# Performance work log

Measured on AMD Instinct MI355X. Metric: run time of the kernel, lower is better.

The kernel has to match this reference:

```python
import math
import jax, jax.numpy as jnp
import numpy as np

B, T, C, H = 2, 4096, 512, 8  # batch, seq_len, n_embd, n_head
D = C // H                    # head_dim = 64

def setup_inputs() -> dict:
    key = jax.random.key(0)
    k1, k2, k3 = jax.random.split(key, 3)
    x = jax.random.normal(k1, (B, T, C), dtype=jnp.float32)
    # torch Linear(C, 3C, bias=False): y = x @ W.T; we store the transposed
    # weight directly so the forward is x @ W_attn.
    W_attn = jax.random.normal(k2, (C, 3 * C), dtype=jnp.float32) * 0.02
    W_proj = jax.random.normal(k3, (C, C), dtype=jnp.float32) * 0.02
    return {"x": x, "W_attn": W_attn, "W_proj": W_proj}

def reference(x, W_attn, W_proj):
    b, t, c = x.shape
    # fused QKV projection, split like .split(n_embd, dim=2)
    qkv = x @ W_attn                              # [B,T,3C]
    q, k, v = jnp.split(qkv, 3, axis=-1)          # each [B,T,C]
    def to_heads(u):
        return u.reshape(b, t, H, D).transpose(0, 2, 1, 3)  # [B,H,T,D]
    q, k, v = to_heads(q), to_heads(k), to_heads(v)
    scale = 1.0 / math.sqrt(D)
    att = jnp.einsum('bhqd,bhkd->bhqk', q, k) * scale       # [B,H,T,T]
    causal = jnp.tril(jnp.ones((t, t), dtype=bool))         # masked_fill(triu(...,1), -inf)
    att = jnp.where(causal, att, -jnp.inf)
    probs = jax.nn.softmax(att, axis=-1)
    y = jnp.einsum('bhqk,bhkd->bhqd', probs, v)             # [B,H,T,D]
    y = y.transpose(0, 2, 1, 3).reshape(b, t, c)            # [B,T,C]
    return y @ W_proj
```

## Files before the change

kernel.cpp:

```cpp
#include <hip/hip_runtime.h>
#include <hip/hip_bf16.h>
#include <stdint.h>


typedef __attribute__((ext_vector_type(8))) short short8;
typedef __attribute__((ext_vector_type(4))) float floatx4;

__device__ __forceinline__ unsigned short f2bf(float f) {
    unsigned int x = __float_as_uint(f);
    unsigned int r = x + 0x7fffu + ((x >> 16) & 1u);
    return (unsigned short)(r >> 16);
}

__global__ __launch_bounds__(256) void convert_x(
    const float* __restrict__ x, unsigned short* __restrict__ xb)
{
    size_t i = ((size_t)blockIdx.x * 256 + threadIdx.x) * 8;
    float4 a = *reinterpret_cast<const float4*>(x + i);
    float4 b = *reinterpret_cast<const float4*>(x + i + 4);
    unsigned short o[8] = {f2bf(a.x), f2bf(a.y), f2bf(a.z), f2bf(a.w),
                           f2bf(b.x), f2bf(b.y), f2bf(b.z), f2bf(b.w)};
    *reinterpret_cast<uint4*>(xb + i) = *reinterpret_cast<uint4*>(o);
}

__global__ __launch_bounds__(256) void transpose_w(
    const float* __restrict__ W, unsigned short* __restrict__ Wt, int Kdim, int Ndim)
{
    __shared__ unsigned short tile[32][34];
    const int tid = threadIdx.x;
    const int tx = tid & 31, ty = tid >> 5;
    const int n0 = blockIdx.x * 32, k0 = blockIdx.y * 32;
    #pragma unroll
    for (int p = 0; p < 4; ++p) {
        int k = k0 + ty + p * 8;
        tile[tx][ty + p * 8] = f2bf(W[(size_t)k * Ndim + n0 + tx]);
    }
    __syncthreads();
    #pragma unroll
    for (int p = 0; p < 4; ++p) {
        int n = n0 + ty + p * 8;
        Wt[(size_t)n * Kdim + k0 + tx] = tile[ty + p * 8][tx];
    }
}

template<int EPI>
__global__ __launch_bounds__(256) void mm_bt(
    const unsigned short* __restrict__ A,
    const unsigned short* __restrict__ Bt,
    void* __restrict__ outp)
{
    __shared__ __align__(16) unsigned short Al[128][40];
    __shared__ __align__(16) unsigned short Bl[128][40];

    const int tid  = threadIdx.x;
    const int wave = tid >> 6;
    const int lane = tid & 63;
    const int quad = lane >> 4;
    const int l16  = lane & 15;
    const int wr   = wave >> 1;
    const int wc   = wave & 1;
    const int n0 = blockIdx.x * 128;
    const int m0 = blockIdx.y * 128;

    floatx4 acc[4][4];
    #pragma unroll
    for (int i = 0; i < 4; ++i)
        #pragma unroll
        for (int j = 0; j < 4; ++j) acc[i][j] = (floatx4){0.f, 0.f, 0.f, 0.f};

    const int row = tid >> 1;
    const int cb  = (tid & 1) * 16;

    const unsigned short* ap = &A[(size_t)(m0 + row) * 512 + cb];
    const unsigned short* bp = &Bt[(size_t)(n0 + row) * 512 + cb];

    uint4 ra0 = *reinterpret_cast<const uint4*>(ap);
    uint4 ra1 = *reinterpret_cast<const uint4*>(ap + 8);
    uint4 rb0 = *reinterpret_cast<const uint4*>(bp);
    uint4 rb1 = *reinterpret_cast<const uint4*>(bp + 8);

    for (int k0 = 0; k0 < 512; k0 += 32) {
        __syncthreads();
        *reinterpret_cast<uint4*>(&Al[row][cb])     = ra0;
        *reinterpret_cast<uint4*>(&Al[row][cb + 8]) = ra1;
        *reinterpret_cast<uint4*>(&Bl[row][cb])     = rb0;
        *reinterpret_cast<uint4*>(&Bl[row][cb + 8]) = rb1;
        __syncthreads();

        if (k0 < 480) {
            ra0 = *reinterpret_cast<const uint4*>(ap + k0 + 32);
            ra1 = *reinterpret_cast<const uint4*>(ap + k0 + 40);
            rb0 = *reinterpret_cast<const uint4*>(bp + k0 + 32);
            rb1 = *reinterpret_cast<const uint4*>(bp + k0 + 40);
        }

        short8 af[4], bf[4];
        #pragma unroll
        for (int ti = 0; ti < 4; ++ti)
            af[ti] = *reinterpret_cast<const short8*>(&Al[wr * 64 + ti * 16 + l16][quad * 8]);
        #pragma unroll
        for (int tj = 0; tj < 4; ++tj)
            bf[tj] = *reinterpret_cast<const short8*>(&Bl[wc * 64 + tj * 16 + l16][quad * 8]);
        #pragma unroll
        for (int ti = 0; ti < 4; ++ti)
            #pragma unroll
            for (int tj = 0; tj < 4; ++tj)
                acc[ti][tj] = __builtin_amdgcn_mfma_f32_16x16x32_bf16(af[ti], bf[tj], acc[ti][tj], 0, 0, 0);
    }

    if (EPI == 0) {
        unsigned short* WS = (unsigned short*)outp;
        unsigned short* Qb  = WS;
        unsigned short* Kb  = WS + 4194304;
        unsigned short* Vtb = WS + 8388608;
        const int which = n0 >> 9;
        const int h = ((n0 + wc * 64) >> 6) & 7;
        const float sc = (which == 0) ? 0.18033688f : 1.0f;
        #pragma unroll
        for (int ti = 0; ti < 4; ++ti) {
            #pragma unroll
            for (int r = 0; r < 4; ++r) {
                int m = m0 + wr * 64 + ti * 16 + quad * 4 + r;
                int b = m >> 12, t = m & 4095;
                int bh = b * 8 + h;
                #pragma unroll
                for (int tj = 0; tj < 4; ++tj) {
                    int d = tj * 16 + l16;
                    unsigned short val = f2bf(acc[ti][tj][r] * sc);
                    if (which == 0)      Qb[((size_t)bh * 4096 + t) * 64 + d] = val;
                    else if (which == 1) Kb[((size_t)bh * 4096 + t) * 64 + d] = val;
                    else                 Vtb[((size_t)bh * 64 + d) * 4096 + t] = val;
                }
            }
        }
    } else {
        float* Out = (float*)outp;
        #pragma unroll
        for (int ti = 0; ti < 4; ++ti) {
            #pragma unroll
            for (int r = 0; r < 4; ++r) {
                int m = m0 + wr * 64 + ti * 16 + quad * 4 + r;
                #pragma unroll
                for (int tj = 0; tj < 4; ++tj) {
                    int n = n0 + wc * 64 + tj * 16 + l16;
                    Out[(size_t)m * 512 + n] = acc[ti][tj][r];
                }
            }
        }
    }
}

__global__ __launch_bounds__(256) void attn_mfma(
    const unsigned short* __restrict__ Q,
    const unsigned short* __restrict__ K,
    const unsigned short* __restrict__ Vt,
    unsigned short* __restrict__ Y)
{
    __shared__ __align__(16) unsigned short Kc[64][72];
    __shared__ __align__(16) unsigned short Vc[64][72];
    __shared__ __align__(16) unsigned short Pc[4][32][72];

    const int tid  = threadIdx.x;
    const int wave = tid >> 6;
    const int lane = tid & 63;
    const int quad = lane >> 4;
    const int l16  = lane & 15;

    const int bid = blockIdx.x;
    const int bh = bid & 15;
    const int j  = (bid >> 4) & 15;
    const int g  = bid >> 8;
    const int qb = g ? (31 - j) : j;
    const int m0 = qb * 128;

    const unsigned short* Qp = Q  + (size_t)bh * (4096 * 64);
    const unsigned short* Kp = K  + (size_t)bh * (4096 * 64);
    const unsigned short* Vp = Vt + (size_t)bh * (64 * 4096);

    short8 qf[2][2];
    #pragma unroll
    for (int h = 0; h < 2; ++h) {
        int qrow = m0 + wave * 32 + h * 16 + l16;
        qf[h][0] = *reinterpret_cast<const short8*>(&Qp[(size_t)qrow * 64 + quad * 8]);
        qf[h][1] = *reinterpret_cast<const short8*>(&Qp[(size_t)qrow * 64 + 32 + quad * 8]);
    }

    short8 ones;
    #pragma unroll
    for (int i = 0; i < 8; ++i) ones[i] = (short)0x3F80;

    floatx4 o[2][4];
    #pragma unroll
    for (int h = 0; h < 2; ++h)
        #pragma unroll
        for (int n = 0; n < 4; ++n) o[h][n] = (floatx4){0.f, 0.f, 0.f, 0.f};
    floatx4 o4[2] = {{0,0,0,0},{0,0,0,0}};

    const int r0 = tid >> 3, c0 = (tid & 7) * 8;
    const int r1 = r0 + 32,  c1 = c0;
    const int ktmax = 2 * qb + 1;
    const int wq0 = m0 + wave * 32;

    uint4 rk0 = *reinterpret_cast<const uint4*>(&Kp[(size_t)r0 * 64 + c0]);
    uint4 rk1 = *reinterpret_cast<const uint4*>(&Kp[(size_t)r1 * 64 + c1]);
    uint4 rv0 = *reinterpret_cast<const uint4*>(&Vp[(size_t)r0 * 4096 + c0]);
    uint4 rv1 = *reinterpret_cast<const uint4*>(&Vp[(size_t)r1 * 4096 + c1]);

    for (int kt = 0; kt <= ktmax; ++kt) {
        __syncthreads();
        *reinterpret_cast<uint4*>(&Kc[r0][c0]) = rk0;
        *reinterpret_cast<uint4*>(&Kc[r1][c1]) = rk1;
        *reinterpret_cast<uint4*>(&Vc[r0][c0]) = rv0;
        *reinterpret_cast<uint4*>(&Vc[r1][c1]) = rv1;
        __syncthreads();

        if (kt < ktmax) {
            const int jn = (kt + 1) * 64;
            rk0 = *reinterpret_cast<const uint4*>(&Kp[(size_t)(jn + r0) * 64 + c0]);
            rk1 = *reinterpret_cast<const uint4*>(&Kp[(size_t)(jn + r1) * 64 + c1]);
            rv0 = *reinterpret_cast<const uint4*>(&Vp[(size_t)r0 * 4096 + jn + c0]);
            rv1 = *reinterpret_cast<const uint4*>(&Vp[(size_t)r1 * 4096 + jn + c1]);
        }

        if (kt * 64 > wq0 + 31) continue;

        float sv[2][4][4];
        #pragma unroll
        for (int ct = 0; ct < 4; ++ct) {
            short8 a0 = *reinterpret_cast<const short8*>(&Kc[ct * 16 + l16][quad * 8]);
            short8 a1 = *reinterpret_cast<const short8*>(&Kc[ct * 16 + l16][32 + quad * 8]);
            floatx4 s0 = {0, 0, 0, 0}, s1 = {0, 0, 0, 0};
            s0 = __builtin_amdgcn_mfma_f32_16x16x32_bf16(a0, qf[0][0], s0, 0, 0, 0);
            s0 = __builtin_amdgcn_mfma_f32_16x16x32_bf16(a1, qf[0][1], s0, 0, 0, 0);
            s1 = __builtin_amdgcn_mfma_f32_16x16x32_bf16(a0, qf[1][0], s1, 0, 0, 0);
            s1 = __builtin_amdgcn_mfma_f32_16x16x32_bf16(a1, qf[1][1], s1, 0, 0, 0);
            #pragma unroll
            for (int r = 0; r < 4; ++r) { sv[0][ct][r] = s0[r]; sv[1][ct][r] = s1[r]; }
        }

        if (kt * 64 + 63 > wq0) {
            #pragma unroll
            for (int h = 0; h < 2; ++h)
                #pragma unroll
                for (int ct = 0; ct < 4; ++ct)
                    #pragma unroll
                    for (int r = 0; r < 4; ++r) {
                        int key = kt * 64 + ct * 16 + quad * 4 + r;
                        int q   = wq0 + h * 16 + l16;
                        sv[h][ct][r] = (key <= q) ? sv[h][ct][r] : -1e30f;
                    }
        }
        #pragma unroll
        for (int h = 0; h < 2; ++h)
            #pragma unroll
            for (int ct = 0; ct < 4; ++ct)
                #pragma unroll
                for (int r = 0; r < 4; ++r)
                    sv[h][ct][r] = __builtin_amdgcn_exp2f(sv[h][ct][r]);

        #pragma unroll
        for (int h = 0; h < 2; ++h)
            #pragma unroll
            for (int ct = 0; ct < 4; ++ct) {
                unsigned int d0 = (unsigned int)f2bf(sv[h][ct][0]) | ((unsigned int)f2bf(sv[h][ct][1]) << 16);
                unsigned int d1 = (unsigned int)f2bf(sv[h][ct][2]) | ((unsigned int)f2bf(sv[h][ct][3]) << 16);
                *reinterpret_cast<uint2*>(&Pc[wave][h * 16 + l16][ct * 16 + quad * 4]) = make_uint2(d0, d1);
            }

        short8 pa[2][2];
        #pragma unroll
        for (int h = 0; h < 2; ++h) {
            pa[h][0] = *reinterpret_cast<const short8*>(&Pc[wave][h * 16 + l16][quad * 8]);
            pa[h][1] = *reinterpret_cast<const short8*>(&Pc[wave][h * 16 + l16][32 + quad * 8]);
        }

        #pragma unroll
        for (int h = 0; h < 2; ++h) {
            o4[h] = __builtin_amdgcn_mfma_f32_16x16x32_bf16(pa[h][0], ones, o4[h], 0, 0, 0);
            o4[h] = __builtin_amdgcn_mfma_f32_16x16x32_bf16(pa[h][1], ones, o4[h], 0, 0, 0);
        }
        #pragma unroll
        for (int n = 0; n < 4; ++n) {
            short8 b0 = *reinterpret_cast<const short8*>(&Vc[n * 16 + l16][quad * 8]);
            short8 b1 = *reinterpret_cast<const short8*>(&Vc[n * 16 + l16][32 + quad * 8]);
            #pragma unroll
            for (int h = 0; h < 2; ++h) {
                o[h][n] = __builtin_amdgcn_mfma_f32_16x16x32_bf16(pa[h][0], b0, o[h][n], 0, 0, 0);
                o[h][n] = __builtin_amdgcn_mfma_f32_16x16x32_bf16(pa[h][1], b1, o[h][n], 0, 0, 0);
            }
        }
    }

    const int b = bh >> 3, h8 = bh & 7;
    #pragma unroll
    for (int h = 0; h < 2; ++h)
        #pragma unroll
        for (int r = 0; r < 4; ++r) {
            float inv = 1.0f / o4[h][r];
            int t = wq0 + h * 16 + quad * 4 + r;
            #pragma unroll
            for (int n = 0; n < 4; ++n)
                Y[((size_t)(b * 4096 + t)) * 512 + h8 * 64 + n * 16 + l16] = f2bf(o[h][n][r] * inv);
        }
}

extern "C" void kernel_launch(void* const* d_in, const int* in_sizes, int n_in,
                              void* d_out, int out_size, void* d_ws, size_t ws_size,
                              hipStream_t stream) {
    const float* x  = (const float*)d_in[0];
    const float* Wa = (const float*)d_in[1];
    const float* Wp = (const float*)d_in[2];
    float* out = (float*)d_out;
    unsigned short* ws = (unsigned short*)d_ws;

    unsigned short* Qb  = ws;
    unsigned short* Kb  = ws + 4194304;
    unsigned short* Vtb = ws + 8388608;
    unsigned short* Yb  = ws + 12582912;
    unsigned short* WaT = Yb;
    unsigned short* WpT = Qb;
    unsigned short* xb  = (unsigned short*)d_out;

    dim3 blk(256);
    convert_x<<<dim3(2048), blk, 0, stream>>>(x, xb);
    transpose_w<<<dim3(48, 16), blk, 0, stream>>>(Wa, WaT, 512, 1536);
    mm_bt<0><<<dim3(12, 64), blk, 0, stream>>>(xb, WaT, (void*)ws);
    attn_mfma<<<dim3(512), blk, 0, stream>>>(Qb, Kb, Vtb, Yb);
    transpose_w<<<dim3(16, 16), blk, 0, stream>>>(Wp, WpT, 512, 512);
    mm_bt<1><<<dim3(4, 64), blk, 0, stream>>>(Yb, WpT, (void*)out);
}
```

Before: 196.4 us.

## Fuse prep kernels, stage V-transpose via LDS, and shrink attention blocks to 64 queries

The x conversion and W_attn transpose are merged into one launch. The QKV GEMM grid is reordered so M varies fastest, and the V epilogue now transposes through shared memory to write coalesced 16-byte rows instead of scattered 2-byte stores. Attention blocks drop to 2 waves covering 64 queries, giving 1024 blocks with the longest-first ordering. Each wave then does only useful key tiles, with masking confined to the diagonal tile. The costs are a larger LDS footprint for the QKV GEMM and more K/V reloads per query across the smaller blocks.

```diff
diff --git a/kernel.cpp b/kernel.cpp
--- a/kernel.cpp
+++ b/kernel.cpp
@@ -12,35 +12,48 @@
     return (unsigned short)(r >> 16);
 }
 
-__global__ __launch_bounds__(256) void convert_x(
-    const float* __restrict__ x, unsigned short* __restrict__ xb)
+__global__ __launch_bounds__(256) void prep_a(
+    const float* __restrict__ x, unsigned short* __restrict__ xb,
+    const float* __restrict__ Wa, unsigned short* __restrict__ WaT)
 {
-    size_t i = ((size_t)blockIdx.x * 256 + threadIdx.x) * 8;
-    float4 a = *reinterpret_cast<const float4*>(x + i);
-    float4 b = *reinterpret_cast<const float4*>(x + i + 4);
-    unsigned short o[8] = {f2bf(a.x), f2bf(a.y), f2bf(a.z), f2bf(a.w),
-                           f2bf(b.x), f2bf(b.y), f2bf(b.z), f2bf(b.w)};
-    *reinterpret_cast<uint4*>(xb + i) = *reinterpret_cast<uint4*>(o);
-}
-
-__global__ __launch_bounds__(256) void transpose_w(
-    const float* __restrict__ W, unsigned short* __restrict__ Wt, int Kdim, int Ndim)
+    const int bid = blockIdx.x;
+    const int tid = threadIdx.x;
+    if (bid < 2048) {
+        size_t i = ((size_t)bid * 256 + tid) * 8;
+        float4 a = *reinterpret_cast<const float4*>(x + i);
+        float4 b = *reinterpret_cast<const float4*>(x + i + 4);
+        unsigned short o[8] = {f2bf(a.x), f2bf(a.y), f2bf(a.z), f2bf(a.w),
+                               f2bf(b.x), f2bf(b.y), f2bf(b.z), f2bf(b.w)};
+        *reinterpret_cast<uint4*>(xb + i) = *reinterpret_cast<uint4*>(o);
+    } else {
+        __shared__ unsigned short tile[32][34];
+        const int t2 = bid - 2048;
+        const int n0 = (t2 % 48) * 32, k0 = (t2 / 48) * 32;
+        const int tx = tid & 31, ty = tid >> 5;
+        #pragma unroll
+        for (int p = 0; p < 4; ++p)
+            tile[tx][ty + p * 8] = f2bf(Wa[(size_t)(k0 + ty + p * 8) * 1536 + n0 + tx]);
+        __syncthreads();
+        #pragma unroll
+        for (int p = 0; p < 4; ++p)
+            WaT[(size_t)(n0 + ty + p * 8) * 512 + k0 + tx] = tile[ty + p * 8][tx];
+    }
+}
+
+__global__ __launch_bounds__(256) void transpose_wp(
+    const float* __restrict__ W, unsigned short* __restrict__ Wt)
 {
     __shared__ unsigned short tile[32][34];
     const int tid = threadIdx.x;
     const int tx = tid & 31, ty = tid >> 5;
     const int n0 = blockIdx.x * 32, k0 = blockIdx.y * 32;
     #pragma unroll
-    for (int p = 0; p < 4; ++p) {
-        int k = k0 + ty + p * 8;
-        tile[tx][ty + p * 8] = f2bf(W[(size_t)k * Ndim + n0 + tx]);
-    }
+    for (int p = 0; p < 4; ++p)
+        tile[tx][ty + p * 8] = f2bf(W[(size_t)(k0 + ty + p * 8) * 512 + n0 + tx]);
     __syncthreads();
     #pragma unroll
-    for (int p = 0; p < 4; ++p) {
-        int n = n0 + ty + p * 8;
-        Wt[(size_t)n * Kdim + k0 + tx] = tile[ty + p * 8][tx];
-    }
+    for (int p = 0; p < 4; ++p)
+        Wt[(size_t)(n0 + ty + p * 8) * 512 + k0 + tx] = tile[ty + p * 8][tx];
 }
 
 template<int EPI>
@@ -49,8 +62,9 @@
     const unsigned short* __restrict__ Bt,
     void* __restrict__ outp)
 {
-    __shared__ __align__(16) unsigned short Al[128][40];
-    __shared__ __align__(16) unsigned short Bl[128][40];
+    __shared__ __align__(16) unsigned char smem[EPI == 0 ? 40960 : 20480];
+    auto Al = reinterpret_cast<unsigned short(*)[40]>(smem);
+    auto Bl = reinterpret_cast<unsigned short(*)[40]>(smem + 10240);
 
     const int tid  = threadIdx.x;
     const int wave = tid >> 6;
@@ -59,8 +73,8 @@
     const int l16  = lane & 15;
     const int wr   = wave >> 1;
     const int wc   = wave & 1;
-    const int n0 = blockIdx.x * 128;
-    const int m0 = blockIdx.y * 128;
+    const int m0 = blockIdx.x * 128;
+    const int n0 = blockIdx.y * 128;
 
     floatx4 acc[4][4];
     #pragma unroll
@@ -115,21 +129,47 @@
         unsigned short* Vtb = WS + 8388608;
         const int which = n0 >> 9;
         const int h = ((n0 + wc * 64) >> 6) & 7;
-        const float sc = (which == 0) ? 0.18033688f : 1.0f;
-        #pragma unroll
-        for (int ti = 0; ti < 4; ++ti) {
-            #pragma unroll
-            for (int r = 0; r < 4; ++r) {
-                int m = m0 + wr * 64 + ti * 16 + quad * 4 + r;
-                int b = m >> 12, t = m & 4095;
-                int bh = b * 8 + h;
+
+        if (which == 2) {
+            auto Tr = reinterpret_cast<unsigned short(*)[80]>(smem);
+            __syncthreads();
+            #pragma unroll
+            for (int ti = 0; ti < 4; ++ti)
                 #pragma unroll
                 for (int tj = 0; tj < 4; ++tj) {
-                    int d = tj * 16 + l16;
-                    unsigned short val = f2bf(acc[ti][tj][r] * sc);
-                    if (which == 0)      Qb[((size_t)bh * 4096 + t) * 64 + d] = val;
-                    else if (which == 1) Kb[((size_t)bh * 4096 + t) * 64 + d] = val;
-                    else                 Vtb[((size_t)bh * 64 + d) * 4096 + t] = val;
+                    unsigned int lo = (unsigned int)f2bf(acc[ti][tj][0]) |
+                                      ((unsigned int)f2bf(acc[ti][tj][1]) << 16);
+                    unsigned int hi = (unsigned int)f2bf(acc[ti][tj][2]) |
+                                      ((unsigned int)f2bf(acc[ti][tj][3]) << 16);
+                    *reinterpret_cast<uint2*>(&Tr[(wave << 6) + tj * 16 + l16][ti * 16 + quad * 4])
+                        = make_uint2(lo, hi);
+                }
+            const int b = m0 >> 12;
+            const int bh = b * 8 + h;
+            const int t0g = (m0 & 4095) + wr * 64;
+            const int tseg = (lane & 7) * 8;
+            #pragma unroll
+            for (int p = 0; p < 8; ++p) {
+                int dl = p * 8 + (lane >> 3);
+                uint4 v = *reinterpret_cast<const uint4*>(&Tr[(wave << 6) + dl][tseg]);
+                *reinterpret_cast<uint4*>(&Vtb[((size_t)(bh * 64 + dl)) * 4096 + t0g + tseg]) = v;
+            }
+        } else {
+            const float sc = (which == 0) ? 0.18033688f : 1.0f;
+            #pragma unroll
+            for (int ti = 0; ti < 4; ++ti) {
+                #pragma unroll
+                for (int r = 0; r < 4; ++r) {
+                    int m = m0 + wr * 64 + ti * 16 + quad * 4 + r;
+                    int b = m >> 12, t = m & 4095;
+                    int bh = b * 8 + h;
+                    #pragma unroll
+                    for (int tj = 0; tj < 4; ++tj) {
+                        int d = tj * 16 + l16;
+                        unsigned short val = f2bf(acc[ti][tj][r] * sc);
+                        if (which == 0) Qb[((size_t)bh * 4096 + t) * 64 + d] = val;
+                        else            Kb[((size_t)bh * 4096 + t) * 64 + d] = val;
+                    }
                 }
             }
         }
@@ -150,7 +190,7 @@
     }
 }
 
-__global__ __launch_bounds__(256) void attn_mfma(
+__global__ __launch_bounds__(128) void attn_mfma(
     const unsigned short* __restrict__ Q,
     const unsigned short* __restrict__ K,
     const unsigned short* __restrict__ Vt,
@@ -158,7 +198,7 @@
 {
     __shared__ __align__(16) unsigned short Kc[64][72];
     __shared__ __align__(16) unsigned short Vc[64][72];
-    __shared__ __align__(16) unsigned short Pc[4][32][72];
+    __shared__ __align__(16) unsigned short Pc[2][32][72];
 
     const int tid  = threadIdx.x;
     const int wave = tid >> 6;
@@ -168,19 +208,19 @@
 
     const int bid = blockIdx.x;
     const int bh = bid & 15;
-    const int j  = (bid >> 4) & 15;
-    const int g  = bid >> 8;
-    const int qb = g ? (31 - j) : j;
-    const int m0 = qb * 128;
+    const int qb = 63 - (bid >> 4);
+    const int m0 = qb * 64;
 
     const unsigned short* Qp = Q  + (size_t)bh * (4096 * 64);
     const unsigned short* Kp = K  + (size_t)bh * (4096 * 64);
     const unsigned short* Vp = Vt + (size_t)bh * (64 * 4096);
 
+    const int wq0 = m0 + wave * 32;
+
     short8 qf[2][2];
     #pragma unroll
     for (int h = 0; h < 2; ++h) {
-        int qrow = m0 + wave * 32 + h * 16 + l16;
+        int qrow = wq0 + h * 16 + l16;
         qf[h][0] = *reinterpret_cast<const short8*>(&Qp[(size_t)qrow * 64 + quad * 8]);
         qf[h][1] = *reinterpret_cast<const short8*>(&Qp[(size_t)qrow * 64 + 32 + quad * 8]);
     }
@@ -196,33 +236,33 @@
         for (int n = 0; n < 4; ++n) o[h][n] = (floatx4){0.f, 0.f, 0.f, 0.f};
     floatx4 o4[2] = {{0,0,0,0},{0,0,0,0}};
 
-    const int r0 = tid >> 3, c0 = (tid & 7) * 8;
-    const int r1 = r0 + 32,  c1 = c0;
-    const int ktmax = 2 * qb + 1;
-    const int wq0 = m0 + wave * 32;
-
-    uint4 rk0 = *reinterpret_cast<const uint4*>(&Kp[(size_t)r0 * 64 + c0]);
-    uint4 rk1 = *reinterpret_cast<const uint4*>(&Kp[(size_t)r1 * 64 + c1]);
-    uint4 rv0 = *reinterpret_cast<const uint4*>(&Vp[(size_t)r0 * 4096 + c0]);
-    uint4 rv1 = *reinterpret_cast<const uint4*>(&Vp[(size_t)r1 * 4096 + c1]);
-
-    for (int kt = 0; kt <= ktmax; ++kt) {
-        __syncthreads();
-        *reinterpret_cast<uint4*>(&Kc[r0][c0]) = rk0;
-        *reinterpret_cast<uint4*>(&Kc[r1][c1]) = rk1;
-        *reinterpret_cast<uint4*>(&Vc[r0][c0]) = rv0;
-        *reinterpret_cast<uint4*>(&Vc[r1][c1]) = rv1;
-        __syncthreads();
-
-        if (kt < ktmax) {
+    const int r0 = tid >> 3;
+    const int c0 = (tid & 7) * 8;
+
+    uint4 rk[4], rv[4];
+    #pragma unroll
+    for (int p = 0; p < 4; ++p) {
+        rk[p] = *reinterpret_cast<const uint4*>(&Kp[(size_t)(r0 + p * 16) * 64 + c0]);
+        rv[p] = *reinterpret_cast<const uint4*>(&Vp[(size_t)(r0 + p * 16) * 4096 + c0]);
+    }
+
+    for (int kt = 0; kt <= qb; ++kt) {
+        __syncthreads();
+        #pragma unroll
+        for (int p = 0; p < 4; ++p) {
+            *reinterpret_cast<uint4*>(&Kc[r0 + p * 16][c0]) = rk[p];
+            *reinterpret_cast<uint4*>(&Vc[r0 + p * 16][c0]) = rv[p];
+        }
+        __syncthreads();
+
+        if (kt < qb) {
             const int jn = (kt + 1) * 64;
-            rk0 = *reinterpret_cast<const uint4*>(&Kp[(size_t)(jn + r0) * 64 + c0]);
-            rk1 = *reinterpret_cast<const uint4*>(&Kp[(size_t)(jn + r1) * 64 + c1]);
-            rv0 = *reinterpret_cast<const uint4*>(&Vp[(size_t)r0 * 4096 + jn + c0]);
-            rv1 = *reinterpret_cast<const uint4*>(&Vp[(size_t)r1 * 4096 + jn + c1]);
-        }
-
-        if (kt * 64 > wq0 + 31) continue;
+            #pragma unroll
+            for (int p = 0; p < 4; ++p) {
+                rk[p] = *reinterpret_cast<const uint4*>(&Kp[(size_t)(jn + r0 + p * 16) * 64 + c0]);
+                rv[p] = *reinterpret_cast<const uint4*>(&Vp[(size_t)(r0 + p * 16) * 4096 + jn + c0]);
+            }
+        }
 
         float sv[2][4][4];
         #pragma unroll
@@ -238,7 +278,7 @@
             for (int r = 0; r < 4; ++r) { sv[0][ct][r] = s0[r]; sv[1][ct][r] = s1[r]; }
         }
 
-        if (kt * 64 + 63 > wq0) {
+        if (kt == qb) {
             #pragma unroll
             for (int h = 0; h < 2; ++h)
                 #pragma unroll
@@ -321,11 +361,9 @@
     unsigned short* WpT = Qb;
     unsigned short* xb  = (unsigned short*)d_out;
 
-    dim3 blk(256);
-    convert_x<<<dim3(2048), blk, 0, stream>>>(x, xb);
-    transpose_w<<<dim3(48, 16), blk, 0, stream>>>(Wa, WaT, 512, 1536);
-    mm_bt<0><<<dim3(12, 64), blk, 0, stream>>>(xb, WaT, (void*)ws);
-    attn_mfma<<<dim3(512), blk, 0, stream>>>(Qb, Kb, Vtb, Yb);
-    transpose_w<<<dim3(16, 16), blk, 0, stream>>>(Wp, WpT, 512, 512);
-    mm_bt<1><<<dim3(4, 64), blk, 0, stream>>>(Yb, WpT, (void*)out);
-}
+    prep_a<<<dim3(2816), dim3(256), 0, stream>>>(x, xb, Wa, WaT);
+    mm_bt<0><<<dim3(64, 12), dim3(256), 0, stream>>>(xb, WaT, (void*)ws);
+    attn_mfma<<<dim3(1024), dim3(128), 0, stream>>>(Qb, Kb, Vtb, Yb);
+    transpose_wp<<<dim3(16, 16), dim3(256), 0, stream>>>(Wp, WpT);
+    mm_bt<1><<<dim3(64, 4), dim3(256), 0, stream>>>(Yb, WpT, (void*)out);
+}
```

Result: slower. 292.7 us (+49.0%).
